# Kernel tuning notes

Hardware: AMD Instinct MI355X
Metric: run time of the kernel (lower is better)

Reference implementation:

```python
import jax, jax.numpy as jnp
import numpy as np

EPS = 1e-6  # NORM_SMALL


def ln(x, scale, bias):
    m = jnp.mean(x, axis=-1, keepdims=True)
    v = jnp.var(x, axis=-1, keepdims=True)
    return (x - m) * jax.lax.rsqrt(v + EPS) * scale + bias


def setup_inputs() -> dict:
    A, C, CP, H = 1024, 128, 128, 8
    key = jax.random.key(0)
    ks = jax.random.split(key, 16)
    inp = {
        "atom_act": jax.random.normal(ks[0], (A, C), jnp.float32),
        "pair_act": jax.random.normal(ks[1], (A, A, CP), jnp.float32),
        "atom_mask": jnp.ones((A,), jnp.float32),
        "pair_mask": jnp.ones((A, A), jnp.float32),
        # query_norm / feat_2d_norm / mat_norm params
        "qn_s": jnp.ones((C,), jnp.float32), "qn_b": jnp.zeros((C,), jnp.float32),
        "f2n_s": jnp.ones((CP,), jnp.float32), "f2n_b": jnp.zeros((CP,), jnp.float32),
        "mn_s": jnp.ones((C,), jnp.float32), "mn_b": jnp.zeros((C,), jnp.float32),
        # pair bias dense (c_pair -> num_head)
        "w2d": jax.random.normal(ks[2], (CP, H), jnp.float32) * (CP ** -0.5),
        # hyper-attention pair matrix dense (c_pair -> atom_act_dim)
        "w_pm": jax.random.normal(ks[3], (CP, C), jnp.float32) * 0.02,
        "b_pm": jnp.zeros((C,), jnp.float32),
        # attention projections
        "wq": jax.random.normal(ks[4], (C, C), jnp.float32) * (C ** -0.5),
        "wk": jax.random.normal(ks[5], (C, C), jnp.float32) * (C ** -0.5),
        "wv": jax.random.normal(ks[6], (C, C), jnp.float32) * (C ** -0.5),
        "wg": jax.random.normal(ks[7], (C, C), jnp.float32) * 0.02,
        "bg": jnp.ones((C,), jnp.float32),
        "wo": jax.random.normal(ks[8], (C, C), jnp.float32) * (C ** -0.5),
        "bo": jnp.zeros((C,), jnp.float32),
    }
    return inp


def reference(atom_act, pair_act, atom_mask, pair_mask,
              qn_s, qn_b, f2n_s, f2n_b, mn_s, mn_b,
              w2d, w_pm, b_pm, wq, wk, wv, wg, bg, wo, bo):
    A, C = atom_act.shape
    H = w2d.shape[1]
    kph = C // H  # key dim per head

    # pre-norm of atom activations (query_norm)
    x = ln(atom_act, qn_s, qn_b)  # [A, C]

    # pair features: norm -> head bias [H, A, A]
    p = ln(pair_act, f2n_s, f2n_b)  # [A, A, CP]
    pair_bias = jnp.transpose(jnp.einsum('ijc,ch->ijh', p, w2d), (2, 0, 1))

    # hyper-attention affine mixing of q/k acts
    pm = pair_mask[..., None]  # [A, A, 1]
    pair_matrix = ln(jnp.einsum('ijc,cd->ijd', p, w_pm) + b_pm, mn_s, mn_b)  # [A, A, C]
    u = jnp.sum(pair_matrix * pm, axis=1) / (jnp.sum(pm, axis=1) + EPS)  # [A, C]
    vmix = jnp.sum(pair_matrix * pm, axis=0) / (jnp.sum(pm, axis=0) + EPS)  # [A, C]
    query_act = x + x * u
    key_act = x + x * vmix

    # attention (bias from atom_mask is computed upstream but unused in Attention)
    q = (query_act @ wq) * (kph ** -0.5)
    k = key_act @ wk
    v = key_act @ wv
    q = q.reshape(A, H, kph)
    k = k.reshape(A, H, kph)
    v = v.reshape(A, H, kph)
    logits = jnp.einsum('ihk,jhk->hij', q, k) + pair_bias  # [H, A, A]
    probs = jax.nn.softmax(logits, axis=-1)
    wa = jnp.einsum('hij,jhk->ihk', probs, v)  # [A, H, kph]
    gate = jax.nn.sigmoid(query_act @ wg + bg).reshape(A, H, kph)
    wa = wa * gate
    out = wa.reshape(A, C) @ wo + bo
    return out
```

## Files before the change

### kernel.cpp

```cpp
#include <hip/hip_runtime.h>
#include <math.h>

constexpr float EPSF = 1e-6f;

typedef __attribute__((ext_vector_type(8))) short short8;
typedef __attribute__((ext_vector_type(4))) float f32x4;

static __device__ __forceinline__ short f2bf(float f) {
    unsigned u = __builtin_bit_cast(unsigned, f);
    u += 0x7FFF + ((u >> 16) & 1);
    return (short)(u >> 16);
}

__global__ __launch_bounds__(256, 1)
void k1_pair(const float* __restrict__ pair_act, const float* __restrict__ pair_mask,
             const float* __restrict__ f2n_s, const float* __restrict__ f2n_b,
             const float* __restrict__ mn_s, const float* __restrict__ mn_b,
             const float* __restrict__ w2d, const float* __restrict__ w_pm,
             const float* __restrict__ b_pm,
             float* __restrict__ pbias,
             float* __restrict__ u_part,
             float* __restrict__ v_part)
{
    __shared__ __align__(16) char As[64 * 256];
    __shared__ __align__(16) char Bt[144 * 256];
    __shared__ float u_sh[64 * 128];

    const int tid = threadIdx.x;
    const int m = tid >> 6;
    const int lane = tid & 63;
    const int cpart = lane & 15;
    const int q = lane >> 4;
    const int it = blockIdx.x >> 4, jt = blockIdx.x & 15;
    const int i0 = it << 6;
    const int j0 = jt << 6;

    for (int idx = tid; idx < 144 * 128; idx += 256) {
        int col = idx >> 7, k = idx & 127;
        float w;
        if (col < 128)       w = w_pm[k * 128 + col];
        else if (col < 136)  w = w2d[k * 8 + (col - 128)];
        else                 w = 0.f;
        int byte = col * 256 + ((2 * k) ^ ((col & 7) << 4));
        *(short*)(Bt + byte) = f2bf(w);
    }
    for (int idx = tid; idx < 2048; idx += 256)
        ((f32x4*)u_sh)[idx] = (f32x4){0.f, 0.f, 0.f, 0.f};
    __syncthreads();

    short8 bfr[9][4];
#pragma unroll
    for (int n = 0; n < 9; n++) {
#pragma unroll
        for (int kk = 0; kk < 4; kk++) {
            int col = n * 16 + cpart;
            int off = (kk * 64 + q * 16) ^ ((col & 7) << 4);
            bfr[n][kk] = *(const short8*)(Bt + col * 256 + off);
        }
    }

    float f2s[8], f2b[8];
#pragma unroll
    for (int v = 0; v < 8; v++) {
        f2s[v] = f2n_s[cpart * 8 + v];
        f2b[v] = f2n_b[cpart * 8 + v];
    }
    float mns[8], mnb[8], bp[8];
#pragma unroll
    for (int n = 0; n < 8; n++) {
        mns[n] = mn_s[n * 16 + cpart];
        mnb[n] = mn_b[n * 16 + cpart];
        bp[n]  = b_pm[n * 16 + cpart];
    }

    float vx[8][4];
#pragma unroll
    for (int n = 0; n < 8; n++)
#pragma unroll
        for (int jj = 0; jj < 4; jj++) vx[n][jj] = 0.f;

    const int arow = m * 16 + cpart;
    const int jrow0 = j0 + m * 16 + q * 4;

    float4 ldA[4][2], ldB[4][2];
#pragma unroll
    for (int t = 0; t < 4; t++) {
        int row_l = m * 16 + t * 4 + q;
        const float4* src = (const float4*)(pair_act +
            ((size_t)i0 * 1024 + (size_t)(j0 + row_l)) * 128 + cpart * 8);
        ldA[t][0] = src[0];
        ldA[t][1] = src[1];
    }

    for (int ii = 0; ii < 64; ii++) {
        const int i_abs = i0 + ii;

        if (ii < 63) {
#pragma unroll
            for (int t = 0; t < 4; t++) {
                int row_l = m * 16 + t * 4 + q;
                const float4* src = (const float4*)(pair_act +
                    ((size_t)(i_abs + 1) * 1024 + (size_t)(j0 + row_l)) * 128 + cpart * 8);
                ldB[t][0] = src[0];
                ldB[t][1] = src[1];
            }
        }
        float mkv[4];
#pragma unroll
        for (int jj = 0; jj < 4; jj++)
            mkv[jj] = pair_mask[(size_t)i_abs * 1024 + jrow0 + jj];

#pragma unroll
        for (int t = 0; t < 4; t++) {
            int row_l = m * 16 + t * 4 + q;
            float xv[8];
            xv[0] = ldA[t][0].x; xv[1] = ldA[t][0].y; xv[2] = ldA[t][0].z; xv[3] = ldA[t][0].w;
            xv[4] = ldA[t][1].x; xv[5] = ldA[t][1].y; xv[6] = ldA[t][1].z; xv[7] = ldA[t][1].w;
            float s = 0.f, ss = 0.f;
#pragma unroll
            for (int v = 0; v < 8; v++) { s += xv[v]; ss += xv[v] * xv[v]; }
#pragma unroll
            for (int off = 1; off < 16; off <<= 1) {
                s += __shfl_xor(s, off);
                ss += __shfl_xor(ss, off);
            }
            float mean = s * 0.0078125f;
            float rinv = rsqrtf(fmaxf(ss * 0.0078125f - mean * mean, 0.f) + EPSF);
            short hs[8];
#pragma unroll
            for (int v = 0; v < 8; v++)
                hs[v] = f2bf((xv[v] - mean) * rinv * f2s[v] + f2b[v]);
            short8 pk = (short8){hs[0], hs[1], hs[2], hs[3], hs[4], hs[5], hs[6], hs[7]};
            *(short8*)(As + row_l * 256 + ((cpart * 16) ^ ((row_l & 7) << 4))) = pk;
        }

        short8 af[4];
#pragma unroll
        for (int kk = 0; kk < 4; kk++)
            af[kk] = *(const short8*)(As + arow * 256 +
                                      ((kk * 64 + q * 16) ^ ((arow & 7) << 4)));
        f32x4 acc[9];
#pragma unroll
        for (int n = 0; n < 9; n++) acc[n] = (f32x4){0.f, 0.f, 0.f, 0.f};
#pragma unroll
        for (int n = 0; n < 9; n++)
#pragma unroll
            for (int kk = 0; kk < 4; kk++)
                acc[n] = __builtin_amdgcn_mfma_f32_16x16x32_bf16(af[kk], bfr[n][kk], acc[n], 0, 0, 0);

        float mean2[4], rinv2[4];
#pragma unroll
        for (int jj = 0; jj < 4; jj++) {
            float s = 0.f, ss = 0.f;
#pragma unroll
            for (int n = 0; n < 8; n++) {
                float tv = acc[n][jj] + bp[n];
                s += tv; ss += tv * tv;
            }
#pragma unroll
            for (int off = 1; off < 16; off <<= 1) {
                s += __shfl_xor(s, off);
                ss += __shfl_xor(ss, off);
            }
            mean2[jj] = s * 0.0078125f;
            rinv2[jj] = rsqrtf(fmaxf(ss * 0.0078125f - mean2[jj] * mean2[jj], 0.f) + EPSF);
        }
#pragma unroll
        for (int n = 0; n < 8; n++) {
            float up = 0.f;
#pragma unroll
            for (int jj = 0; jj < 4; jj++) {
                float pm = (acc[n][jj] + bp[n] - mean2[jj]) * rinv2[jj] * mns[n] + mnb[n];
                float w = pm * mkv[jj];
                up += w;
                vx[n][jj] += w;
            }
            atomicAdd(&u_sh[ii * 128 + n * 16 + cpart], up);
        }

        if (cpart < 8) {
#pragma unroll
            for (int jj = 0; jj < 4; jj++)
                pbias[(((size_t)i_abs * 8 + cpart) << 10) + jrow0 + jj] = acc[8][jj];
        }

#pragma unroll
        for (int t = 0; t < 4; t++) { ldA[t][0] = ldB[t][0]; ldA[t][1] = ldB[t][1]; }
    }

#pragma unroll
    for (int n = 0; n < 8; n++)
#pragma unroll
        for (int jj = 0; jj < 4; jj++)
            v_part[((size_t)it * 1024 + jrow0 + jj) * 128 + n * 16 + cpart] = vx[n][jj];

    __syncthreads();
    float* ub = &u_part[((size_t)jt * 1024 + i0) * 128];
    for (int idx = tid; idx < 2048; idx += 256)
        ((float4*)ub)[idx] = ((float4*)u_sh)[idx];
}

__global__ __launch_bounds__(256)
void k_rowsum(const float* __restrict__ pm, float* __restrict__ msr) {
    int i = (blockIdx.x << 2) + (threadIdx.x >> 6);
    int lane = threadIdx.x & 63;
    const float4* row = (const float4*)&pm[(size_t)i << 10];
    float s = 0.f;
#pragma unroll
    for (int q = 0; q < 4; q++) {
        float4 v = row[(q << 6) + lane];
        s += v.x + v.y + v.z + v.w;
    }
#pragma unroll
    for (int off = 32; off; off >>= 1) s += __shfl_xor(s, off);
    if (lane == 0) msr[i] = s;
}

__global__ __launch_bounds__(512)
void k_colsum(const float* __restrict__ pm, float* __restrict__ msc) {
    __shared__ float red[512];
    int jb = blockIdx.x << 5;
    int jtl = threadIdx.x & 31, ig = threadIdx.x >> 5;
    float s = 0.f;
    for (int i = ig; i < 1024; i += 16) s += pm[((size_t)i << 10) + jb + jtl];
    red[threadIdx.x] = s;
    __syncthreads();
    for (int st = 8; st > 0; st >>= 1) {
        if (ig < st) red[threadIdx.x] += red[threadIdx.x + (st << 5)];
        __syncthreads();
    }
    if (ig == 0) msc[jb + jtl] = red[jtl];
}

__global__ __launch_bounds__(256)
void k_fin(const float* __restrict__ up, const float* __restrict__ vp,
           const float* __restrict__ msr, const float* __restrict__ msc,
           float* __restrict__ uf, float* __restrict__ vf) {
    int b = blockIdx.x;
    if (b < 512) {
        int idx = (b << 8) + threadIdx.x;
        float s = 0.f;
#pragma unroll
        for (int t = 0; t < 16; t++) s += up[((size_t)t << 17) + idx];
        uf[idx] = s / (msr[idx >> 7] + EPSF);
    } else {
        int idx = ((b - 512) << 8) + threadIdx.x;
        float s = 0.f;
#pragma unroll
        for (int t = 0; t < 16; t++) s += vp[((size_t)t << 17) + idx];
        vf[idx] = s / (msc[idx >> 7] + EPSF);
    }
}

__global__ __launch_bounds__(256)
void k3_act(const float* __restrict__ aa, const float* __restrict__ qns,
            const float* __restrict__ qnb, const float* __restrict__ uf,
            const float* __restrict__ vf, float* __restrict__ qa,
            float* __restrict__ ka) {
    int i = (blockIdx.x << 2) + (threadIdx.x >> 6);
    int lane = threadIdx.x & 63, c0 = lane << 1;
    float2 x2 = *(const float2*)&aa[(i << 7) + c0];
    float s = x2.x + x2.y, ss = x2.x * x2.x + x2.y * x2.y;
#pragma unroll
    for (int off = 32; off; off >>= 1) {
        s += __shfl_xor(s, off);
        ss += __shfl_xor(ss, off);
    }
    float m = s * 0.0078125f;
    float rinv = rsqrtf(fmaxf(ss * 0.0078125f - m * m, 0.f) + EPSF);
    float xa = (x2.x - m) * rinv * qns[c0] + qnb[c0];
    float xb = (x2.y - m) * rinv * qns[c0 + 1] + qnb[c0 + 1];
    float2 u2 = *(const float2*)&uf[(i << 7) + c0];
    float2 v2 = *(const float2*)&vf[(i << 7) + c0];
    *(float2*)&qa[(i << 7) + c0] = make_float2(xa * (1.f + u2.x), xb * (1.f + u2.y));
    *(float2*)&ka[(i << 7) + c0] = make_float2(xa * (1.f + v2.x), xb * (1.f + v2.y));
}

__global__ __launch_bounds__(256)
void k4_proj(const float* __restrict__ qa, const float* __restrict__ ka,
             const float* __restrict__ wq, const float* __restrict__ wk,
             const float* __restrict__ wv, const float* __restrict__ wg,
             const float* __restrict__ bg, float* __restrict__ qh,
             float* __restrict__ kh, float* __restrict__ vT,
             float* __restrict__ gate) {
    __shared__ float Wl[128 * 128];
    __shared__ float inl[16 * 128];
    int m = blockIdx.y, rb = blockIdx.x, t = threadIdx.x;
    const float* W = (m == 0) ? wq : (m == 1) ? wk : (m == 2) ? wv : wg;
    const float* in = (m == 0 || m == 3) ? qa : ka;
#pragma unroll
    for (int k = 0; k < 16; k++)
        ((float4*)Wl)[(k << 8) + t] = ((const float4*)W)[(k << 8) + t];
#pragma unroll
    for (int k = 0; k < 2; k++)
        ((float4*)inl)[(k << 8) + t] = ((const float4*)&in[rb << 11])[(k << 8) + t];
    __syncthreads();

    int c = t & 127, r2 = t >> 7;
    float acc[8] = {0.f, 0.f, 0.f, 0.f, 0.f, 0.f, 0.f, 0.f};
    const float* wcol = &Wl[c];
    const float* ib = &inl[(r2 << 3) * 128];
#pragma unroll 8
    for (int k = 0; k < 128; k++) {
        float wvv = wcol[k << 7];
#pragma unroll
        for (int r = 0; r < 8; r++) acc[r] += ib[(r << 7) + k] * wvv;
    }
    int h = c >> 4, kk = c & 15;
    int row0 = (rb << 4) + (r2 << 3);
    if (m == 0) {
#pragma unroll
        for (int r = 0; r < 8; r++) qh[(h << 14) + ((row0 + r) << 4) + kk] = acc[r] * 0.25f;
    } else if (m == 1) {
#pragma unroll
        for (int r = 0; r < 8; r++) kh[(h << 14) + ((row0 + r) << 4) + kk] = acc[r];
    } else if (m == 2) {
#pragma unroll
        for (int r = 0; r < 8; r++) vT[(h << 14) + (kk << 10) + row0 + r] = acc[r];
    } else {
        float b = bg[c];
#pragma unroll
        for (int r = 0; r < 8; r++)
            gate[((row0 + r) << 7) + c] = 1.f / (1.f + __expf(-(acc[r] + b)));
    }
}

__global__ __launch_bounds__(64)
void k5_attn(const float* __restrict__ qh, const float* __restrict__ kh,
             const float* __restrict__ vT, const float* __restrict__ pbias,
             const float* __restrict__ gate, float* __restrict__ wag) {
    __shared__ float p_lds[1024];
    int b = blockIdx.x;
    int h = b >> 10, i = b & 1023;
    int lane = threadIdx.x;

    const float* qp = &qh[(h << 14) + (i << 4)];
    float ql[16];
#pragma unroll
    for (int kk = 0; kk < 16; kk++) ql[kk] = qp[kk];

    const float* kbase = &kh[h << 14];
    const float* bias = &pbias[(((size_t)i << 3) + h) << 10];

    float lg[16];
    float mx = -1e30f;
#pragma unroll
    for (int jc = 0; jc < 16; jc++) {
        int j = (jc << 6) + lane;
        const float4* kr = (const float4*)&kbase[j << 4];
        float4 ka = kr[0], kb = kr[1], kc = kr[2], kd = kr[3];
        float acc = bias[j];
        acc += ql[0] * ka.x + ql[1] * ka.y + ql[2] * ka.z + ql[3] * ka.w;
        acc += ql[4] * kb.x + ql[5] * kb.y + ql[6] * kb.z + ql[7] * kb.w;
        acc += ql[8] * kc.x + ql[9] * kc.y + ql[10] * kc.z + ql[11] * kc.w;
        acc += ql[12] * kd.x + ql[13] * kd.y + ql[14] * kd.z + ql[15] * kd.w;
        lg[jc] = acc;
        mx = fmaxf(mx, acc);
    }
#pragma unroll
    for (int off = 32; off; off >>= 1) mx = fmaxf(mx, __shfl_xor(mx, off));
    float S = 0.f;
#pragma unroll
    for (int jc = 0; jc < 16; jc++) {
        float p = __expf(lg[jc] - mx);
        S += p;
        p_lds[(jc << 6) + lane] = p;
    }
#pragma unroll
    for (int off = 32; off; off >>= 1) S += __shfl_xor(S, off);
    float inv = 1.f / S;
    __syncthreads();

    int jj = lane >> 4, kk = lane & 15;
    const float* vp = &vT[(h << 14) + (kk << 10)];
    float acc = 0.f;
#pragma unroll 4
    for (int jb = 0; jb < 64; jb++) {
        int j4 = (jb << 4) + (jj << 2);
        float4 p4 = *(const float4*)&p_lds[j4];
        float4 v4 = *(const float4*)&vp[j4];
        acc += p4.x * v4.x + p4.y * v4.y + p4.z * v4.z + p4.w * v4.w;
    }
    acc += __shfl_xor(acc, 16);
    acc += __shfl_xor(acc, 32);
    if (lane < 16) {
        float g = gate[(i << 7) + (h << 4) + kk];
        wag[(i << 7) + (h << 4) + kk] = acc * inv * g;
    }
}

__global__ __launch_bounds__(256)
void k6_out(const float* __restrict__ wag, const float* __restrict__ wo,
            const float* __restrict__ bo, float* __restrict__ out) {
    __shared__ float Wl[128 * 128];
    __shared__ float inl[16 * 128];
    int rb = blockIdx.x, t = threadIdx.x;
#pragma unroll
    for (int k = 0; k < 16; k++)
        ((float4*)Wl)[(k << 8) + t] = ((const float4*)wo)[(k << 8) + t];
#pragma unroll
    for (int k = 0; k < 2; k++)
        ((float4*)inl)[(k << 8) + t] = ((const float4*)&wag[rb << 11])[(k << 8) + t];
    __syncthreads();

    int c = t & 127, r2 = t >> 7;
    float acc[8] = {0.f, 0.f, 0.f, 0.f, 0.f, 0.f, 0.f, 0.f};
    const float* wcol = &Wl[c];
    const float* ib = &inl[(r2 << 3) * 128];
#pragma unroll 8
    for (int k = 0; k < 128; k++) {
        float wvv = wcol[k << 7];
#pragma unroll
        for (int r = 0; r < 8; r++) acc[r] += ib[(r << 7) + k] * wvv;
    }
    int row0 = (rb << 4) + (r2 << 3);
    float b = bo[c];
#pragma unroll
    for (int r = 0; r < 8; r++) out[((row0 + r) << 7) + c] = acc[r] + b;
}

extern "C" void kernel_launch(void* const* d_in, const int* in_sizes, int n_in,
                              void* d_out, int out_size, void* d_ws, size_t ws_size,
                              hipStream_t stream) {
    const float* atom_act  = (const float*)d_in[0];
    const float* pair_act  = (const float*)d_in[1];
    const float* pair_mask = (const float*)d_in[3];
    const float* qn_s = (const float*)d_in[4];
    const float* qn_b = (const float*)d_in[5];
    const float* f2n_s = (const float*)d_in[6];
    const float* f2n_b = (const float*)d_in[7];
    const float* mn_s = (const float*)d_in[8];
    const float* mn_b = (const float*)d_in[9];
    const float* w2d  = (const float*)d_in[10];
    const float* w_pm = (const float*)d_in[11];
    const float* b_pm = (const float*)d_in[12];
    const float* wq = (const float*)d_in[13];
    const float* wk = (const float*)d_in[14];
    const float* wv = (const float*)d_in[15];
    const float* wg = (const float*)d_in[16];
    const float* bg = (const float*)d_in[17];
    const float* wo = (const float*)d_in[18];
    const float* bo = (const float*)d_in[19];

    float* ws = (float*)d_ws;
    float* pbias  = ws;
    float* u_part = pbias + 8 * 1024 * 1024;
    float* v_part = u_part + 16 * 1024 * 128;
    float* msr    = v_part + 16 * 1024 * 128;
    float* msc    = msr + 1024;
    float* uf     = msc + 1024;
    float* vf     = uf + 131072;
    float* qa     = vf + 131072;
    float* ka     = qa + 131072;
    float* qh     = ka + 131072;
    float* kh     = qh + 131072;
    float* vT     = kh + 131072;
    float* gate   = vT + 131072;
    float* wag    = gate + 131072;
    (void)in_sizes; (void)n_in; (void)out_size; (void)ws_size;

    k_rowsum<<<256, 256, 0, stream>>>(pair_mask, msr);
    k_colsum<<<32, 512, 0, stream>>>(pair_mask, msc);
    k1_pair<<<256, 256, 0, stream>>>(pair_act, pair_mask, f2n_s, f2n_b, mn_s, mn_b,
                                     w2d, w_pm, b_pm, pbias, u_part, v_part);
    k_fin<<<1024, 256, 0, stream>>>(u_part, v_part, msr, msc, uf, vf);
    k3_act<<<256, 256, 0, stream>>>(atom_act, qn_s, qn_b, uf, vf, qa, ka);
    k4_proj<<<dim3(64, 4), 256, 0, stream>>>(qa, ka, wq, wk, wv, wg, bg, qh, kh, vT, gate);
    k5_attn<<<8192, 64, 0, stream>>>(qh, kh, vT, pbias, gate, wag);
    k6_out<<<64, 256, 0, stream>>>(wag, wo, bo, (float*)d_out);
}
```

Baseline: 1.058 ms.

## Alias u accumulator onto weight LDS, raise occupancy, reduce atomics via shuffles

The u accumulation buffer now reuses the LDS region that held the transposed weights once they are in registers, which cuts shared memory use, and launch bounds go from 1 to 2 blocks per CU. Partial u sums are first reduced across the four lane quads with shuffles, so only one quarter of the lanes issue LDS atomics. Mask values are prefetched one row ahead as a float4, and the pair-bias output is written as a float4. Asking for 2 blocks per CU caps the register budget, which may force spills given the large register arrays (bfr, vx, acc).

```diff
diff --git a/kernel.cpp b/kernel.cpp
--- a/kernel.cpp
+++ b/kernel.cpp
@@ -12,7 +12,7 @@
     return (short)(u >> 16);
 }
 
-__global__ __launch_bounds__(256, 1)
+__global__ __launch_bounds__(256, 2)
 void k1_pair(const float* __restrict__ pair_act, const float* __restrict__ pair_mask,
              const float* __restrict__ f2n_s, const float* __restrict__ f2n_b,
              const float* __restrict__ mn_s, const float* __restrict__ mn_b,
@@ -23,8 +23,7 @@
              float* __restrict__ v_part)
 {
     __shared__ __align__(16) char As[64 * 256];
-    __shared__ __align__(16) char Bt[144 * 256];
-    __shared__ float u_sh[64 * 128];
+    __shared__ __align__(16) char BtU[144 * 256];
 
     const int tid = threadIdx.x;
     const int m = tid >> 6;
@@ -42,10 +41,8 @@
         else if (col < 136)  w = w2d[k * 8 + (col - 128)];
         else                 w = 0.f;
         int byte = col * 256 + ((2 * k) ^ ((col & 7) << 4));
-        *(short*)(Bt + byte) = f2bf(w);
-    }
-    for (int idx = tid; idx < 2048; idx += 256)
-        ((f32x4*)u_sh)[idx] = (f32x4){0.f, 0.f, 0.f, 0.f};
+        *(short*)(BtU + byte) = f2bf(w);
+    }
     __syncthreads();
 
     short8 bfr[9][4];
@@ -55,9 +52,16 @@
         for (int kk = 0; kk < 4; kk++) {
             int col = n * 16 + cpart;
             int off = (kk * 64 + q * 16) ^ ((col & 7) << 4);
-            bfr[n][kk] = *(const short8*)(Bt + col * 256 + off);
-        }
-    }
+            bfr[n][kk] = *(const short8*)(BtU + col * 256 + off);
+        }
+    }
+    __syncthreads();
+
+    float* u_sh = (float*)BtU;
+#pragma unroll
+    for (int k = 0; k < 8; k++)
+        ((f32x4*)u_sh)[tid + (k << 8)] = (f32x4){0.f, 0.f, 0.f, 0.f};
+    __syncthreads();
 
     float f2s[8], f2b[8];
 #pragma unroll
@@ -83,6 +87,7 @@
     const int jrow0 = j0 + m * 16 + q * 4;
 
     float4 ldA[4][2], ldB[4][2];
+    float4 mkA, mkB;
 #pragma unroll
     for (int t = 0; t < 4; t++) {
         int row_l = m * 16 + t * 4 + q;
@@ -91,6 +96,7 @@
         ldA[t][0] = src[0];
         ldA[t][1] = src[1];
     }
+    mkA = *(const float4*)&pair_mask[(size_t)i0 * 1024 + jrow0];
 
     for (int ii = 0; ii < 64; ii++) {
         const int i_abs = i0 + ii;
@@ -104,11 +110,9 @@
                 ldB[t][0] = src[0];
                 ldB[t][1] = src[1];
             }
-        }
-        float mkv[4];
-#pragma unroll
-        for (int jj = 0; jj < 4; jj++)
-            mkv[jj] = pair_mask[(size_t)i_abs * 1024 + jrow0 + jj];
+            mkB = *(const float4*)&pair_mask[(size_t)(i_abs + 1) * 1024 + jrow0];
+        }
+        const float mkv[4] = {mkA.x, mkA.y, mkA.z, mkA.w};
 
 #pragma unroll
         for (int t = 0; t < 4; t++) {
@@ -165,27 +169,38 @@
             mean2[jj] = s * 0.0078125f;
             rinv2[jj] = rsqrtf(fmaxf(ss * 0.0078125f - mean2[jj] * mean2[jj], 0.f) + EPSF);
         }
+        float up[8];
 #pragma unroll
         for (int n = 0; n < 8; n++) {
-            float up = 0.f;
+            float u_acc = 0.f;
 #pragma unroll
             for (int jj = 0; jj < 4; jj++) {
                 float pm = (acc[n][jj] + bp[n] - mean2[jj]) * rinv2[jj] * mns[n] + mnb[n];
                 float w = pm * mkv[jj];
-                up += w;
+                u_acc += w;
                 vx[n][jj] += w;
             }
-            atomicAdd(&u_sh[ii * 128 + n * 16 + cpart], up);
+            up[n] = u_acc;
+        }
+#pragma unroll
+        for (int n = 0; n < 8; n++) {
+            up[n] += __shfl_xor(up[n], 16);
+            up[n] += __shfl_xor(up[n], 32);
+        }
+        if (q == 0) {
+#pragma unroll
+            for (int n = 0; n < 8; n++)
+                atomicAdd(&u_sh[(ii << 7) + n * 16 + cpart], up[n]);
         }
 
         if (cpart < 8) {
-#pragma unroll
-            for (int jj = 0; jj < 4; jj++)
-                pbias[(((size_t)i_abs * 8 + cpart) << 10) + jrow0 + jj] = acc[8][jj];
+            *(float4*)&pbias[(((size_t)i_abs * 8 + cpart) << 10) + jrow0] =
+                *(float4*)&acc[8];
         }
 
 #pragma unroll
         for (int t = 0; t < 4; t++) { ldA[t][0] = ldB[t][0]; ldA[t][1] = ldB[t][1]; }
+        mkA = mkB;
     }
 
 #pragma unroll
```

New measurement: 1.474 ms. +39.3%, slower.
